# Kernel optimization log

Measured on AMD Instinct MI355X. Metric: run time of the kernel, lower is better.

Reference implementation:

```python
import jax, jax.numpy as jnp
import numpy as np

PATCH_SIZE = 128
NUM_PATCHES = 4


def setup_inputs() -> dict:
    key = jax.random.key(0)
    k1, k2 = jax.random.split(key)
    B, C, H, W = 32, 3, 512, 512
    images = jax.random.normal(k1, (B, C, H, W), dtype=jnp.float32)
    uncertainty_maps = jax.random.uniform(k2, (B, 1, H, W), dtype=jnp.float32)
    return {"images": images, "uncertainty_maps": uncertainty_maps}


def _select_patches(umap):
    """Greedy masked-argmax patch selection on one [H, W] uncertainty map.
    Returns coords [NUM_PATCHES, 4] int32 as (x1, y1, x2, y2)."""
    H, W = umap.shape
    eps = min(PATCH_SIZE, H // 2, W // 2)   # effective patch size (static)
    half = eps // 2
    margin = max(eps // 4, 1)
    ys = jnp.arange(H)[:, None]
    xs = jnp.arange(W)[None, :]

    def fix(a1, a2, L):
        # enforce window of exactly `eps` when clipped at the border
        small = (a2 - a1) < eps
        a2n = jnp.where(a1 == 0, jnp.minimum(L, a1 + eps), a2)
        a1n = jnp.where(a1 == 0, a1, jnp.maximum(0, a2 - eps))
        return jnp.where(small, a1n, a1), jnp.where(small, a2n, a2)

    def step(mask, _):
        masked = jnp.where(mask, -jnp.inf, umap)
        idx = jnp.argmax(masked)            # row-major first-max, same as np.ma.argmax
        yc = idx // W
        xc = idx % W
        x1 = jnp.maximum(0, xc - half)
        x2 = jnp.minimum(W, xc + half)
        y1 = jnp.maximum(0, yc - half)
        y2 = jnp.minimum(H, yc + half)
        x1, x2 = fix(x1, x2, W)
        y1, y2 = fix(y1, y2, H)
        # suppress selected region plus margin (clamping implicit in comparisons)
        box = (ys >= y1 - margin) & (ys < y2 + margin) & (xs >= x1 - margin) & (xs < x2 + margin)
        coords = jnp.stack([x1, y1, x2, y2]).astype(jnp.int32)
        return mask | box, coords

    _, coords = jax.lax.scan(step, jnp.zeros((H, W), dtype=bool), None, length=NUM_PATCHES)
    return coords  # [NUM_PATCHES, 4]


def _extract(images, coords):
    B, C, H, W = images.shape
    eps = min(PATCH_SIZE, H // 2, W // 2)

    def crop_one(img, c):
        # img [C,H,W], c = (x1,y1,x2,y2); window is always exactly eps x eps
        p = jax.lax.dynamic_slice(img, (0, c[1], c[0]), (C, eps, eps))
        if eps != PATCH_SIZE:
            # bilinear, matches F.interpolate(align_corners=False)
            p = jax.image.resize(p, (C, PATCH_SIZE, PATCH_SIZE), method="bilinear")
        return p

    return jax.vmap(jax.vmap(crop_one, in_axes=(None, 0)), in_axes=(0, 0))(images, coords)


def reference(images, uncertainty_maps):
    coords = jax.vmap(_select_patches)(uncertainty_maps[:, 0])   # [B, N, 4] int32
    patches = _extract(images, coords)                           # [B, N, C, P, P]
    return patches, coords.astype(jnp.float32)
```

## Files before the change

kernel.cpp:

```cpp
#include <hip/hip_runtime.h>
#include <math.h>
#include <float.h>

#define BN 32
#define CH 3
#define HH 512
#define WW 512
#define NP 4
#define EPS 128
#define HALF 64
#define MARGIN 32

#define NT 4096
#define PATCH_ELEMS (BN * NP * CH * EPS * EPS)
#define F4_PER_MAP (NP * CH * EPS * EPS / 4)
#define NSLICE 16
#define F4_PER_SLICE (F4_PER_MAP / NSLICE)
#define K1_NTHR 256
#define K1_NBLK (BN * NT / K1_NTHR)
#define EX_NBLK (BN * NSLICE)

__global__ __launch_bounds__(K1_NTHR)
void tile_scan(const float* __restrict__ umaps, float2* __restrict__ tiles)
{
    const int g  = blockIdx.x * K1_NTHR + threadIdx.x;
    const int b  = g >> 12;
    const int t  = g & (NT - 1);
    const int tx = t & 63, ty = t >> 6;
    const float* __restrict__ um = umaps + (size_t)b * HH * WW;
    const int x0 = tx << 3, y0 = ty << 3;
    float bv = -INFINITY; int bi = 0x7fffffff;
    #pragma unroll
    for (int r = 0; r < 8; ++r) {
        const int rowbase = (y0 + r) * WW + x0;
        const float4 a = *(const float4*)(um + rowbase);
        const float4 c = *(const float4*)(um + rowbase + 4);
        if (a.x > bv) { bv = a.x; bi = rowbase + 0; }
        if (a.y > bv) { bv = a.y; bi = rowbase + 1; }
        if (a.z > bv) { bv = a.z; bi = rowbase + 2; }
        if (a.w > bv) { bv = a.w; bi = rowbase + 3; }
        if (c.x > bv) { bv = c.x; bi = rowbase + 4; }
        if (c.y > bv) { bv = c.y; bi = rowbase + 5; }
        if (c.z > bv) { bv = c.z; bi = rowbase + 6; }
        if (c.w > bv) { bv = c.w; bi = rowbase + 7; }
    }
    tiles[g] = make_float2(bv, __int_as_float(bi));
}

__global__ __launch_bounds__(1024)
void select_k(const float* __restrict__ umaps,
              const float2* __restrict__ tiles,
              float* __restrict__ out,
              int2* __restrict__ sxy)
{
    const int tid  = threadIdx.x;
    const int lane = tid & 63;
    const int wave = tid >> 6;
    const int b    = blockIdx.x;
    const float* __restrict__ um = umaps + (size_t)b * HH * WW;
    float* coords_out = out + PATCH_ELEMS;

    __shared__ float2   tvi[NT];
    __shared__ float2   l2[64];
    __shared__ unsigned dirty[128];
    __shared__ int      boxes[NP][4];

    {
        const float4* __restrict__ src = (const float4*)(tiles + (size_t)b * NT);
        float4* dst = (float4*)tvi;
        dst[tid]        = src[tid];
        dst[tid + 1024] = src[tid + 1024];
    }
    if (tid < 128) dirty[tid] = 0u;
    if (tid < NP) { boxes[tid][0] = 0; boxes[tid][1] = 0; boxes[tid][2] = 0; boxes[tid][3] = 0; }
    __syncthreads();

    for (int r = wave; r < 64; r += 16) {
        const float2 e = tvi[(r << 6) + lane];
        float v = e.x; int ix = __float_as_int(e.y);
        #pragma unroll
        for (int off = 32; off > 0; off >>= 1) {
            const float ov = __shfl_down(v, off);
            const int   oi = __shfl_down(ix, off);
            if (ov > v || (ov == v && oi < ix)) { v = ov; ix = oi; }
        }
        if (lane == 0) l2[r] = make_float2(v, __int_as_float(ix));
    }
    __syncthreads();

    for (int k = 0; k < NP; ++k) {
        if (wave == 0) {
            for (;;) {
                const float2 e = l2[lane];
                float v = e.x; int ix = __float_as_int(e.y);
                #pragma unroll
                for (int off = 32; off > 0; off >>= 1) {
                    const float ov = __shfl_down(v, off);
                    const int   oi = __shfl_down(ix, off);
                    if (ov > v || (ov == v && oi < ix)) { v = ov; ix = oi; }
                }
                ix = __shfl(ix, 0);
                const int t = ((ix >> 12) << 6) | ((ix & 511) >> 3);
                const bool isdirty = (dirty[t >> 5] >> (t & 31)) & 1u;
                if (!isdirty) {
                    if (lane == 0) {
                        const int yc = ix >> 9, xc = ix & 511;
                        int x1 = max(0, xc - HALF), x2 = min(WW, xc + HALF);
                        int y1 = max(0, yc - HALF), y2 = min(HH, yc + HALF);
                        if (x2 - x1 < EPS) { if (x1 == 0) x2 = EPS; else x1 = x2 - EPS; }
                        if (y2 - y1 < EPS) { if (y1 == 0) y2 = EPS; else y1 = y2 - EPS; }
                        boxes[k][0] = max(x1 - MARGIN, 0);
                        boxes[k][1] = min(x2 + MARGIN, WW);
                        boxes[k][2] = max(y1 - MARGIN, 0);
                        boxes[k][3] = min(y2 + MARGIN, HH);
                        const int o = (b * NP + k) * 4;
                        coords_out[o + 0] = (float)x1;
                        coords_out[o + 1] = (float)y1;
                        coords_out[o + 2] = (float)x2;
                        coords_out[o + 3] = (float)y2;
                        sxy[b * NP + k] = make_int2(x1, y1);
                    }
                    break;
                }
                const int ty = t >> 6, tx = t & 63;
                const int y = (ty << 3) + (lane >> 3), x = (tx << 3) + (lane & 7);
                float pv = um[y * WW + x];
                int   pi = y * WW + x;
                bool m = false;
                #pragma unroll
                for (int j = 0; j < NP; ++j)
                    m |= (y >= boxes[j][2] && y < boxes[j][3] &&
                          x >= boxes[j][0] && x < boxes[j][1]);
                if (m) { pv = -INFINITY; pi = 0x7fffffff; }
                float nv = pv; int ni = pi;
                #pragma unroll
                for (int off = 32; off > 0; off >>= 1) {
                    const float ov = __shfl_down(nv, off);
                    const int   oi = __shfl_down(ni, off);
                    if (ov > nv || (ov == nv && oi < ni)) { nv = ov; ni = oi; }
                }
                nv = __shfl(nv, 0); ni = __shfl(ni, 0);
                if (lane == 0) {
                    tvi[t] = make_float2(nv, __int_as_float(ni));
                    dirty[t >> 5] &= ~(1u << (t & 31));
                }
                const float2 e2 = tvi[(ty << 6) + lane];
                float rv; int ri;
                if (lane == tx) { rv = nv; ri = ni; }
                else            { rv = e2.x; ri = __float_as_int(e2.y); }
                #pragma unroll
                for (int off = 32; off > 0; off >>= 1) {
                    const float ov = __shfl_down(rv, off);
                    const int   oi = __shfl_down(ri, off);
                    if (ov > rv || (ov == rv && oi < ri)) { rv = ov; ri = oi; }
                }
                if (lane == 0) l2[ty] = make_float2(rv, __int_as_float(ri));
            }
        }
        __syncthreads();

        if (k == NP - 1) break;

        const int ex1 = boxes[k][0], ex2 = boxes[k][1];
        const int ey1 = boxes[k][2], ey2 = boxes[k][3];
        const int tx1 = ex1 >> 3, tx2 = (ex2 - 1) >> 3;
        const int ty1 = ey1 >> 3, ty2 = (ey2 - 1) >> 3;
        const int wt  = tx2 - tx1 + 1;
        const int nt2 = wt * (ty2 - ty1 + 1);
        if (tid < nt2) {
            const int tx = tx1 + tid % wt;
            const int ty = ty1 + tid / wt;
            const int t  = (ty << 6) + tx;
            const int X1 = tx << 3, Y1 = ty << 3;
            if (X1 >= ex1 && X1 + 8 <= ex2 && Y1 >= ey1 && Y1 + 8 <= ey2)
                tvi[t] = make_float2(-INFINITY, __int_as_float(0x7fffffff));
            else
                atomicOr(&dirty[t >> 5], 1u << (t & 31));
        }
        __syncthreads();

        for (int r = ty1 + wave; r <= ty2; r += 16) {
            const float2 e = tvi[(r << 6) + lane];
            float v = e.x; int ix = __float_as_int(e.y);
            #pragma unroll
            for (int off = 32; off > 0; off >>= 1) {
                const float ov = __shfl_down(v, off);
                const int   oi = __shfl_down(ix, off);
                if (ov > v || (ov == v && oi < ix)) { v = ov; ix = oi; }
            }
            if (lane == 0) l2[r] = make_float2(v, __int_as_float(ix));
        }
        __syncthreads();
    }
}

__global__ __launch_bounds__(1024)
void extract_k(const float* __restrict__ images,
               const int2* __restrict__ sxy,
               float* __restrict__ out)
{
    const int tid   = threadIdx.x;
    const int b     = blockIdx.x >> 4;
    const int slice = blockIdx.x & (NSLICE - 1);
    float4* __restrict__ out4 = (float4*)out;

    #pragma unroll
    for (int it = 0; it < 3; ++it) {
        const int il  = slice * F4_PER_SLICE + (it << 10) + tid;
        const int nc  = il >> 12;
        const int n   = nc / 3;
        const int c   = nc - n * 3;
        const int py  = (il >> 5) & 127;
        const int px0 = (il & 31) << 2;

        const int2 xy = sxy[b * NP + n];
        const float* __restrict__ src =
            images + (((size_t)b * CH + c) * HH + (xy.y + py)) * WW + xy.x + px0;
        out4[(size_t)b * F4_PER_MAP + il] = make_float4(src[0], src[1], src[2], src[3]);
    }
}

extern "C" void kernel_launch(void* const* d_in, const int* in_sizes, int n_in,
                              void* d_out, int out_size, void* d_ws, size_t ws_size,
                              hipStream_t stream) {
    const float* images = (const float*)d_in[0];
    const float* umaps  = (const float*)d_in[1];
    float* out          = (float*)d_out;
    float2* tiles       = (float2*)d_ws;
    int2*   sxy         = (int2*)((char*)d_ws + (size_t)BN * NT * sizeof(float2));

    tile_scan<<<K1_NBLK, K1_NTHR, 0, stream>>>(umaps, tiles);
    select_k<<<BN, 1024, 0, stream>>>(umaps, tiles, out, sxy);
    extract_k<<<EX_NBLK, 1024, 0, stream>>>(images, sxy, out);
}
```

Before: 180.4 us.

## Fuse patch selection into extraction with redundant per-slice selection

Merges the selection and extraction kernels into one launch of BN*NSLICE blocks. Each block redoes the greedy selection only up to the patch index it needs, then copies its slice of that patch straight from the images. This drops a kernel launch, the dependency gap between kernels and the sxy round trip through global memory. In exchange selection work is duplicated across 16 blocks per image, and the later patches need more serial greedy steps.

```diff
diff --git a/kernel.cpp b/kernel.cpp
--- a/kernel.cpp
+++ b/kernel.cpp
@@ -18,7 +18,6 @@
 #define F4_PER_SLICE (F4_PER_MAP / NSLICE)
 #define K1_NTHR 256
 #define K1_NBLK (BN * NT / K1_NTHR)
-#define EX_NBLK (BN * NSLICE)
 
 __global__ __launch_bounds__(K1_NTHR)
 void tile_scan(const float* __restrict__ umaps, float2* __restrict__ tiles)
@@ -48,15 +47,17 @@
 }
 
 __global__ __launch_bounds__(1024)
-void select_k(const float* __restrict__ umaps,
-              const float2* __restrict__ tiles,
-              float* __restrict__ out,
-              int2* __restrict__ sxy)
+void select_extract(const float* __restrict__ images,
+                    const float* __restrict__ umaps,
+                    const float2* __restrict__ tiles,
+                    float* __restrict__ out)
 {
-    const int tid  = threadIdx.x;
-    const int lane = tid & 63;
-    const int wave = tid >> 6;
-    const int b    = blockIdx.x;
+    const int tid   = threadIdx.x;
+    const int lane  = tid & 63;
+    const int wave  = tid >> 6;
+    const int b     = blockIdx.x & (BN - 1);
+    const int slice = blockIdx.x >> 5;
+    const int nwant = slice >> 2;
     const float* __restrict__ um = umaps + (size_t)b * HH * WW;
     float* coords_out = out + PATCH_ELEMS;
 
@@ -64,6 +65,7 @@
     __shared__ float2   l2[64];
     __shared__ unsigned dirty[128];
     __shared__ int      boxes[NP][4];
+    __shared__ int      px1, py1;
 
     {
         const float4* __restrict__ src = (const float4*)(tiles + (size_t)b * NT);
@@ -88,7 +90,7 @@
     }
     __syncthreads();
 
-    for (int k = 0; k < NP; ++k) {
+    for (int k = 0; k <= nwant; ++k) {
         if (wave == 0) {
             for (;;) {
                 const float2 e = l2[lane];
@@ -113,12 +115,14 @@
                         boxes[k][1] = min(x2 + MARGIN, WW);
                         boxes[k][2] = max(y1 - MARGIN, 0);
                         boxes[k][3] = min(y2 + MARGIN, HH);
-                        const int o = (b * NP + k) * 4;
-                        coords_out[o + 0] = (float)x1;
-                        coords_out[o + 1] = (float)y1;
-                        coords_out[o + 2] = (float)x2;
-                        coords_out[o + 3] = (float)y2;
-                        sxy[b * NP + k] = make_int2(x1, y1);
+                        if (k == nwant) { px1 = x1; py1 = y1; }
+                        if (slice == NSLICE - 1) {
+                            const int o = (b * NP + k) * 4;
+                            coords_out[o + 0] = (float)x1;
+                            coords_out[o + 1] = (float)y1;
+                            coords_out[o + 2] = (float)x2;
+                            coords_out[o + 3] = (float)y2;
+                        }
                     }
                     break;
                 }
@@ -159,7 +163,7 @@
         }
         __syncthreads();
 
-        if (k == NP - 1) break;
+        if (k == nwant) break;
 
         const int ex1 = boxes[k][0], ex2 = boxes[k][1];
         const int ey1 = boxes[k][2], ey2 = boxes[k][3];
@@ -192,30 +196,19 @@
         }
         __syncthreads();
     }
-}
-
-__global__ __launch_bounds__(1024)
-void extract_k(const float* __restrict__ images,
-               const int2* __restrict__ sxy,
-               float* __restrict__ out)
-{
-    const int tid   = threadIdx.x;
-    const int b     = blockIdx.x >> 4;
-    const int slice = blockIdx.x & (NSLICE - 1);
+
+    const int x1 = px1, y1 = py1;
     float4* __restrict__ out4 = (float4*)out;
-
     #pragma unroll
     for (int it = 0; it < 3; ++it) {
         const int il  = slice * F4_PER_SLICE + (it << 10) + tid;
         const int nc  = il >> 12;
-        const int n   = nc / 3;
-        const int c   = nc - n * 3;
+        const int c   = nc - nwant * 3;
         const int py  = (il >> 5) & 127;
         const int px0 = (il & 31) << 2;
 
-        const int2 xy = sxy[b * NP + n];
         const float* __restrict__ src =
-            images + (((size_t)b * CH + c) * HH + (xy.y + py)) * WW + xy.x + px0;
+            images + (((size_t)b * CH + c) * HH + (y1 + py)) * WW + x1 + px0;
         out4[(size_t)b * F4_PER_MAP + il] = make_float4(src[0], src[1], src[2], src[3]);
     }
 }
@@ -227,9 +220,7 @@
     const float* umaps  = (const float*)d_in[1];
     float* out          = (float*)d_out;
     float2* tiles       = (float2*)d_ws;
-    int2*   sxy         = (int2*)((char*)d_ws + (size_t)BN * NT * sizeof(float2));
 
     tile_scan<<<K1_NBLK, K1_NTHR, 0, stream>>>(umaps, tiles);
-    select_k<<<BN, 1024, 0, stream>>>(umaps, tiles, out, sxy);
-    extract_k<<<EX_NBLK, 1024, 0, stream>>>(images, sxy, out);
+    select_extract<<<BN * NSLICE, 1024, 0, stream>>>(images, umaps, tiles, out);
 }
```

Measured after the change: 173.8 us. 1.04x faster.

## Fuse tile scan into selection via last-block pattern, nontemporal patch stores

Applied to the files above, without the earlier changes.

Merges the tile max scan and the greedy patch selection into one kernel where the last finishing block per image performs selection, using an atomic counter reset by a tiny init kernel. Row-level maxima are computed during the scan and reused, removing the initial per-row reduction. The extract kernel switches to a vector load and nontemporal stores to reduce cache pollution. The selection phase now runs with 256 threads instead of 1024, which may lengthen the serial part.

```diff
diff --git a/kernel.cpp b/kernel.cpp
--- a/kernel.cpp
+++ b/kernel.cpp
@@ -18,45 +18,29 @@
 #define F4_PER_SLICE (F4_PER_MAP / NSLICE)
 #define K1_NTHR 256
 #define K1_NBLK (BN * NT / K1_NTHR)
-#define EX_NBLK (BN * NSLICE)
+
+typedef float f4v __attribute__((ext_vector_type(4), aligned(4)));
+
+
+__global__ void init_k(int* __restrict__ done)
+{
+    if (threadIdx.x < BN) done[threadIdx.x] = 0;
+}
 
 __global__ __launch_bounds__(K1_NTHR)
-void tile_scan(const float* __restrict__ umaps, float2* __restrict__ tiles)
-{
-    const int g  = blockIdx.x * K1_NTHR + threadIdx.x;
-    const int b  = g >> 12;
-    const int t  = g & (NT - 1);
-    const int tx = t & 63, ty = t >> 6;
-    const float* __restrict__ um = umaps + (size_t)b * HH * WW;
-    const int x0 = tx << 3, y0 = ty << 3;
-    float bv = -INFINITY; int bi = 0x7fffffff;
-    #pragma unroll
-    for (int r = 0; r < 8; ++r) {
-        const int rowbase = (y0 + r) * WW + x0;
-        const float4 a = *(const float4*)(um + rowbase);
-        const float4 c = *(const float4*)(um + rowbase + 4);
-        if (a.x > bv) { bv = a.x; bi = rowbase + 0; }
-        if (a.y > bv) { bv = a.y; bi = rowbase + 1; }
-        if (a.z > bv) { bv = a.z; bi = rowbase + 2; }
-        if (a.w > bv) { bv = a.w; bi = rowbase + 3; }
-        if (c.x > bv) { bv = c.x; bi = rowbase + 4; }
-        if (c.y > bv) { bv = c.y; bi = rowbase + 5; }
-        if (c.z > bv) { bv = c.z; bi = rowbase + 6; }
-        if (c.w > bv) { bv = c.w; bi = rowbase + 7; }
-    }
-    tiles[g] = make_float2(bv, __int_as_float(bi));
-}
-
-__global__ __launch_bounds__(1024)
-void select_k(const float* __restrict__ umaps,
-              const float2* __restrict__ tiles,
-              float* __restrict__ out,
-              int2* __restrict__ sxy)
+void scan_select(const float* __restrict__ umaps,
+                 float2* __restrict__ tiles,
+                 float2* __restrict__ l2g,
+                 int* __restrict__ done,
+                 int2* __restrict__ sxy,
+                 float* __restrict__ out)
 {
     const int tid  = threadIdx.x;
     const int lane = tid & 63;
     const int wave = tid >> 6;
-    const int b    = blockIdx.x;
+    const int b    = blockIdx.x >> 4;
+    const int t    = ((blockIdx.x & 15) << 8) + tid;
+    const int tx   = t & 63, ty = t >> 6;
     const float* __restrict__ um = umaps + (size_t)b * HH * WW;
     float* coords_out = out + PATCH_ELEMS;
 
@@ -64,28 +48,56 @@
     __shared__ float2   l2[64];
     __shared__ unsigned dirty[128];
     __shared__ int      boxes[NP][4];
+    __shared__ int      islast;
+
+    {
+        const int x0 = tx << 3, y0 = ty << 3;
+        float bv = -INFINITY; int bi = 0x7fffffff;
+        #pragma unroll
+        for (int r = 0; r < 8; ++r) {
+            const int rowbase = (y0 + r) * WW + x0;
+            const float4 a = *(const float4*)(um + rowbase);
+            const float4 c = *(const float4*)(um + rowbase + 4);
+            if (a.x > bv) { bv = a.x; bi = rowbase + 0; }
+            if (a.y > bv) { bv = a.y; bi = rowbase + 1; }
+            if (a.z > bv) { bv = a.z; bi = rowbase + 2; }
+            if (a.w > bv) { bv = a.w; bi = rowbase + 3; }
+            if (c.x > bv) { bv = c.x; bi = rowbase + 4; }
+            if (c.y > bv) { bv = c.y; bi = rowbase + 5; }
+            if (c.z > bv) { bv = c.z; bi = rowbase + 6; }
+            if (c.w > bv) { bv = c.w; bi = rowbase + 7; }
+        }
+        tiles[b * NT + t] = make_float2(bv, __int_as_float(bi));
+        float rv = bv; int ri = bi;
+        #pragma unroll
+        for (int off = 32; off > 0; off >>= 1) {
+            const float ov = __shfl_down(rv, off);
+            const int   oi = __shfl_down(ri, off);
+            if (ov > rv || (ov == rv && oi < ri)) { rv = ov; ri = oi; }
+        }
+        if (lane == 0) l2g[b * 64 + ty] = make_float2(rv, __int_as_float(ri));
+    }
+
+    __syncthreads();
+    if (tid == 0) {
+        __threadfence();
+        islast = (__hip_atomic_fetch_add(&done[b], 1, __ATOMIC_RELAXED,
+                                         __HIP_MEMORY_SCOPE_AGENT) == 15);
+    }
+    __syncthreads();
+    if (!islast) return;
+    __threadfence();
 
     {
         const float4* __restrict__ src = (const float4*)(tiles + (size_t)b * NT);
         float4* dst = (float4*)tvi;
-        dst[tid]        = src[tid];
-        dst[tid + 1024] = src[tid + 1024];
-    }
+        #pragma unroll
+        for (int i = 0; i < 8; ++i)
+            dst[tid + (i << 8)] = src[tid + (i << 8)];
+    }
+    if (tid < 64)  l2[tid] = l2g[b * 64 + tid];
     if (tid < 128) dirty[tid] = 0u;
-    if (tid < NP) { boxes[tid][0] = 0; boxes[tid][1] = 0; boxes[tid][2] = 0; boxes[tid][3] = 0; }
-    __syncthreads();
-
-    for (int r = wave; r < 64; r += 16) {
-        const float2 e = tvi[(r << 6) + lane];
-        float v = e.x; int ix = __float_as_int(e.y);
-        #pragma unroll
-        for (int off = 32; off > 0; off >>= 1) {
-            const float ov = __shfl_down(v, off);
-            const int   oi = __shfl_down(ix, off);
-            if (ov > v || (ov == v && oi < ix)) { v = ov; ix = oi; }
-        }
-        if (lane == 0) l2[r] = make_float2(v, __int_as_float(ix));
-    }
+    if (tid < NP)  { boxes[tid][0] = 0; boxes[tid][1] = 0; boxes[tid][2] = 0; boxes[tid][3] = 0; }
     __syncthreads();
 
     for (int k = 0; k < NP; ++k) {
@@ -100,8 +112,8 @@
                     if (ov > v || (ov == v && oi < ix)) { v = ov; ix = oi; }
                 }
                 ix = __shfl(ix, 0);
-                const int t = ((ix >> 12) << 6) | ((ix & 511) >> 3);
-                const bool isdirty = (dirty[t >> 5] >> (t & 31)) & 1u;
+                const int tt = ((ix >> 12) << 6) | ((ix & 511) >> 3);
+                const bool isdirty = (dirty[tt >> 5] >> (tt & 31)) & 1u;
                 if (!isdirty) {
                     if (lane == 0) {
                         const int yc = ix >> 9, xc = ix & 511;
@@ -113,17 +125,17 @@
                         boxes[k][1] = min(x2 + MARGIN, WW);
                         boxes[k][2] = max(y1 - MARGIN, 0);
                         boxes[k][3] = min(y2 + MARGIN, HH);
+                        sxy[b * NP + k] = make_int2(x1, y1);
                         const int o = (b * NP + k) * 4;
                         coords_out[o + 0] = (float)x1;
                         coords_out[o + 1] = (float)y1;
                         coords_out[o + 2] = (float)x2;
                         coords_out[o + 3] = (float)y2;
-                        sxy[b * NP + k] = make_int2(x1, y1);
                     }
                     break;
                 }
-                const int ty = t >> 6, tx = t & 63;
-                const int y = (ty << 3) + (lane >> 3), x = (tx << 3) + (lane & 7);
+                const int tyd = tt >> 6, txd = tt & 63;
+                const int y = (tyd << 3) + (lane >> 3), x = (txd << 3) + (lane & 7);
                 float pv = um[y * WW + x];
                 int   pi = y * WW + x;
                 bool m = false;
@@ -141,20 +153,20 @@
                 }
                 nv = __shfl(nv, 0); ni = __shfl(ni, 0);
                 if (lane == 0) {
-                    tvi[t] = make_float2(nv, __int_as_float(ni));
-                    dirty[t >> 5] &= ~(1u << (t & 31));
-                }
-                const float2 e2 = tvi[(ty << 6) + lane];
-                float rv; int ri;
-                if (lane == tx) { rv = nv; ri = ni; }
-                else            { rv = e2.x; ri = __float_as_int(e2.y); }
+                    tvi[tt] = make_float2(nv, __int_as_float(ni));
+                    dirty[tt >> 5] &= ~(1u << (tt & 31));
+                }
+                const float2 e2 = tvi[(tyd << 6) + lane];
+                float rv2; int ri2;
+                if (lane == txd) { rv2 = nv; ri2 = ni; }
+                else             { rv2 = e2.x; ri2 = __float_as_int(e2.y); }
                 #pragma unroll
                 for (int off = 32; off > 0; off >>= 1) {
-                    const float ov = __shfl_down(rv, off);
-                    const int   oi = __shfl_down(ri, off);
-                    if (ov > rv || (ov == rv && oi < ri)) { rv = ov; ri = oi; }
-                }
-                if (lane == 0) l2[ty] = make_float2(rv, __int_as_float(ri));
+                    const float ov = __shfl_down(rv2, off);
+                    const int   oi = __shfl_down(ri2, off);
+                    if (ov > rv2 || (ov == rv2 && oi < ri2)) { rv2 = ov; ri2 = oi; }
+                }
+                if (lane == 0) l2[tyd] = make_float2(rv2, __int_as_float(ri2));
             }
         }
         __syncthreads();
@@ -167,19 +179,19 @@
         const int ty1 = ey1 >> 3, ty2 = (ey2 - 1) >> 3;
         const int wt  = tx2 - tx1 + 1;
         const int nt2 = wt * (ty2 - ty1 + 1);
-        if (tid < nt2) {
-            const int tx = tx1 + tid % wt;
-            const int ty = ty1 + tid / wt;
-            const int t  = (ty << 6) + tx;
-            const int X1 = tx << 3, Y1 = ty << 3;
+        for (int i = tid; i < nt2; i += K1_NTHR) {
+            const int txi = tx1 + i % wt;
+            const int tyi = ty1 + i / wt;
+            const int tt  = (tyi << 6) + txi;
+            const int X1 = txi << 3, Y1 = tyi << 3;
             if (X1 >= ex1 && X1 + 8 <= ex2 && Y1 >= ey1 && Y1 + 8 <= ey2)
-                tvi[t] = make_float2(-INFINITY, __int_as_float(0x7fffffff));
+                tvi[tt] = make_float2(-INFINITY, __int_as_float(0x7fffffff));
             else
-                atomicOr(&dirty[t >> 5], 1u << (t & 31));
+                atomicOr(&dirty[tt >> 5], 1u << (tt & 31));
         }
         __syncthreads();
 
-        for (int r = ty1 + wave; r <= ty2; r += 16) {
+        for (int r = ty1 + wave; r <= ty2; r += 4) {
             const float2 e = tvi[(r << 6) + lane];
             float v = e.x; int ix = __float_as_int(e.y);
             #pragma unroll
@@ -202,7 +214,7 @@
     const int tid   = threadIdx.x;
     const int b     = blockIdx.x >> 4;
     const int slice = blockIdx.x & (NSLICE - 1);
-    float4* __restrict__ out4 = (float4*)out;
+    f4v* __restrict__ out4 = (f4v*)out;
 
     #pragma unroll
     for (int it = 0; it < 3; ++it) {
@@ -216,7 +228,8 @@
         const int2 xy = sxy[b * NP + n];
         const float* __restrict__ src =
             images + (((size_t)b * CH + c) * HH + (xy.y + py)) * WW + xy.x + px0;
-        out4[(size_t)b * F4_PER_MAP + il] = make_float4(src[0], src[1], src[2], src[3]);
+        const f4v v = *(const f4v*)src;
+        __builtin_nontemporal_store(v, &out4[(size_t)b * F4_PER_MAP + il]);
     }
 }
 
@@ -227,9 +240,11 @@
     const float* umaps  = (const float*)d_in[1];
     float* out          = (float*)d_out;
     float2* tiles       = (float2*)d_ws;
-    int2*   sxy         = (int2*)((char*)d_ws + (size_t)BN * NT * sizeof(float2));
-
-    tile_scan<<<K1_NBLK, K1_NTHR, 0, stream>>>(umaps, tiles);
-    select_k<<<BN, 1024, 0, stream>>>(umaps, tiles, out, sxy);
-    extract_k<<<EX_NBLK, 1024, 0, stream>>>(images, sxy, out);
-}
+    float2* l2g         = tiles + (size_t)BN * NT;
+    int*    done        = (int*)(l2g + BN * 64);
+    int2*   sxy         = (int2*)(done + BN);
+
+    init_k<<<1, 64, 0, stream>>>(done);
+    scan_select<<<K1_NBLK, K1_NTHR, 0, stream>>>(umaps, tiles, l2g, done, sxy, out);
+    extract_k<<<BN * NSLICE, 1024, 0, stream>>>(images, sxy, out);
+}
```

Result: slower. 213.9 us (+18.5%).
